# Optimization experiments

Hardware: AMD Instinct MI355X
Metric: run time of the kernel (lower is better)

The kernel has to match this reference:

```python
import jax, jax.numpy as jnp
import numpy as np

P = 10          # num_patches
EPS = 1e-20
ALPHAS = dict(stretch=1.0, E=1.0, G=1.0, skew=1.0, total_area=1.0, total_area_mult=1.0)
ALPHA_MC = 1.0
ALPHA_DISTORT = 1.0


def setup_inputs() -> dict:
    key = jax.random.key(0)
    k1, k2, k3, k4 = jax.random.split(key, 4)
    B, N, M = 8, 8192, 2500
    pc_gt = jax.random.normal(k1, (B, N, 3), dtype=jnp.float32)
    pc_pred = jax.random.normal(k2, (B, M, 3), dtype=jnp.float32)
    # first fundamental form (E, F, G); ensure E*G - F^2 > 0 so sqrt is smooth
    u = jax.random.uniform(k3, (B, M, 3), dtype=jnp.float32)
    fff = u * 0.5 + jnp.array([1.0, 0.0, 1.0], dtype=jnp.float32)
    A_gt = jax.random.uniform(k4, (B,), dtype=jnp.float32)
    return {"pc_gt": pc_gt, "pc_pred": pc_pred, "fff": fff, "A_gt": A_gt}


def _forward(pc_gt, pc_pred, fff, A_gt):
    B, M, _ = pc_pred.shape
    spp = M // P

    # ---- Chamfer distance via dense (B, M, N) distance matrix + argmin ----
    diff = pc_pred[:, :, None, :] - pc_gt[:, None, :, :]          # (B, M, N, 3)
    distm = jnp.sqrt(jnp.sum(diff * diff, axis=3))                # (B, M, N)
    inds_p2gt = jnp.argmin(distm, axis=2)                         # (B, M)
    inds_gt2p = jnp.argmin(distm, axis=1)                         # (B, N)
    pc_gt_reg = jnp.take_along_axis(pc_gt, inds_p2gt[..., None], axis=1)   # (B, M, 3)
    pc_p_reg = jnp.take_along_axis(pc_pred, inds_gt2p[..., None], axis=1)  # (B, N, 3)
    d_p2gt = jnp.sum((pc_pred - pc_gt_reg) ** 2, axis=2)
    d_gt2p = jnp.sum((pc_gt - pc_p_reg) ** 2, axis=2)
    L_chd = d_p2gt.mean() + d_gt2p.mean()

    # ---- FFF-based losses ----
    EFG = jnp.transpose(fff.reshape(B, P, spp, 3), (3, 0, 1, 2))  # (3, B, P, spp)
    E, F, G = EFG[0], EFG[1], EFG[2]

    # metric consistency between consecutive frame pairs
    Eh = E.reshape(B // 2, 2, P, spp)
    Fh = F.reshape(B // 2, 2, P, spp)
    Gh = G.reshape(B // 2, 2, P, spp)
    L_mc = ((Eh[:, 0] - Eh[:, 1]) ** 2
            + 2.0 * (Fh[:, 0] - Fh[:, 1]) ** 2
            + (Gh[:, 0] - Gh[:, 1]) ** 2).mean()

    # scaled isometry (collapse) losses
    A2 = jnp.maximum(E * G - F * F, 0.0)                          # (B, P, spp)
    A = jnp.sqrt(A2)
    inv = 1.0 / (A2 + EPS)
    L_stretch = (((E - G) ** 2) * inv).mean() * ALPHAS['stretch']
    L_E = (((E - E.mean()) ** 2) * inv).mean() * ALPHAS['E']
    L_G = (((G - G.mean()) ** 2) * inv).mean() * ALPHAS['G']
    L_F = ((F * F) * inv).mean() * ALPHAS['skew']

    # overlap / total-area loss
    A_tot = A.mean(axis=2).sum(axis=1)                            # (B,)
    L_olap = (jnp.maximum(0.0, A_tot - A_gt * ALPHAS['total_area_mult']) ** 2).mean() * ALPHAS['total_area']

    loss_sciso = L_F + L_E + L_G + L_stretch + L_olap
    loss_tot = L_chd + ALPHA_MC * L_mc + ALPHA_DISTORT * loss_sciso
    return loss_tot


def reference(pc_gt, pc_pred, fff, A_gt):
    return _forward(pc_gt, pc_pred, fff, A_gt)
```

## Files before the change

kernel.cpp:

```cpp
#include <hip/hip_runtime.h>

#define B_   8
#define N_   8192
#define M_   2500
#define SPP_ 250
#define EPS_ 1e-20f
#define BIGF 1e30f

#define NB_P2GT 320
#define NB_GT2P 256
#define NB_FFF  79
#define NB_K1   (NB_P2GT + NB_GT2P + NB_FFF)

#define NB_RG2P 256
#define NB_RP2  79
#define NB_K2   (NB_RG2P + NB_RP2)

#define WS_P2GT 0
#define WS_GT2P 160000
#define WS_ACC  291072
#define WS_RED  291092
#define WS_CNT  291427
#define A_E    0
#define A_G    1
#define A_MC   2
#define A_ST   3
#define A_F2I  4
#define A_E2I  5
#define A_EI   6
#define A_G2I  7
#define A_GI   8
#define A_I    9
#define A_AB   10
#define RO_G2P 0
#define RO_P2  256

typedef __attribute__((ext_vector_type(8))) short short8_t;
typedef __attribute__((ext_vector_type(4))) float float4_t;

__device__ __forceinline__ unsigned pack_bf2(float lo, float hi) {
    unsigned a = __float_as_uint(lo);
    unsigned b = __float_as_uint(hi);
    a = (a + 0x7FFFu + ((a >> 16) & 1u)) >> 16;
    b = (b + 0x7FFFu + ((b >> 16) & 1u)) & 0xFFFF0000u;
    return a | b;
}
__device__ __forceinline__ short bf16s(float x) {
    unsigned a = __float_as_uint(x);
    return (short)((a + 0x7FFFu + ((a >> 16) & 1u)) >> 16);
}
__device__ __forceinline__ float wave_sum64(float v) {
    #pragma unroll
    for (int o = 32; o > 0; o >>= 1) v += __shfl_down(v, o, 64);
    return v;
}
__device__ __forceinline__ float block_sum256(float v, volatile float* red4) {
    v = wave_sum64(v);
    int wid = threadIdx.x >> 6, lane = threadIdx.x & 63;
    if (lane == 0) red4[wid] = v;
    __syncthreads();
    float r = 0.f;
    if (threadIdx.x == 0) r = red4[0] + red4[1] + red4[2] + red4[3];
    __syncthreads();
    return r;
}
__device__ __forceinline__ void min4(float4_t& c, const float4_t d) {
    c.x = fminf(c.x, d.x); c.y = fminf(c.y, d.y);
    c.z = fminf(c.z, d.z); c.w = fminf(c.w, d.w);
}
__device__ __forceinline__ void quad_min4(float4_t& c) {
    #pragma unroll
    for (int m = 1; m < 16; m <<= 1) {
        c.x = fminf(c.x, __shfl_xor(c.x, m, 64));
        c.y = fminf(c.y, __shfl_xor(c.y, m, 64));
        c.z = fminf(c.z, __shfl_xor(c.z, m, 64));
        c.w = fminf(c.w, __shfl_xor(c.w, m, 64));
    }
}

__global__ void __launch_bounds__(256, 2) k1_main(
        const float* __restrict__ gt, const float* __restrict__ pred,
        const float* __restrict__ fff, float* __restrict__ ws) {
    __shared__ uint4 spts[1280];
    __shared__ __align__(16) float saux[516];
    const int bid = blockIdx.x;
    const int tid = threadIdx.x;
    const int lane = tid & 63;
    const int w    = tid >> 6;
    const int quad = lane >> 4;
    const int l15  = lane & 15;
    float* acc = ws + WS_ACC;

    if (bid == 0 && tid == 0) ((unsigned*)(ws + WS_CNT))[0] = 0u;

    if (bid < NB_P2GT + NB_GT2P) {
        const bool is_p2gt = bid < NB_P2GT;
        int b, mblk, z, ntiles, blim, alim;
        const float* apts; const float* bpts; float* dst;
        if (is_p2gt) {
            z = bid / 40; int rem = bid % 40;
            b = rem / 5;  mblk = rem % 5;
            apts = pred + (size_t)b * M_ * 3;
            bpts = gt + ((size_t)b * N_ + (size_t)z * 1024) * 3;
            ntiles = 64; blim = 1024; alim = M_;
            dst = ws + WS_P2GT + (size_t)z * 20000 + b * M_;
        } else {
            int r = bid - NB_P2GT;
            z = r >> 7; int rem = r & 127;
            b = rem >> 4; mblk = rem & 15;
            apts = gt + (size_t)b * N_ * 3;
            bpts = pred + ((size_t)b * M_ + (size_t)z * 1280) * 3;
            ntiles = 80; blim = M_ - z * 1280; alim = N_;
            dst = ws + WS_GT2P + (size_t)z * 65536 + b * N_;
        }
        const int abase = mblk * 512;
        const int nstage = ntiles * 16;

        for (int i = tid; i < nstage; i += 256) {
            float x = 0.f, y = 0.f, zc = 0.f, n2 = BIGF;
            if (i < blim) {
                x = bpts[i * 3 + 0]; y = bpts[i * 3 + 1]; zc = bpts[i * 3 + 2];
                n2 = x * x + y * y + zc * zc;
            }
            uint4 q;
            q.x = pack_bf2(-2.f * x, -2.f * y);
            q.y = pack_bf2(-2.f * zc, n2);
            q.z = q.x; q.w = q.y;
            spts[i] = q;
        }

        short8_t af[8];
        #pragma unroll
        for (int t = 0; t < 8; ++t) af[t] = (short8_t){0,0,0,0,0,0,0,0};
        if (lane < 16) {
            #pragma unroll
            for (int t = 0; t < 8; ++t) {
                int m = abase + w * 128 + t * 16 + l15;
                int c = m < alim ? m : alim - 1;
                float x = apts[c*3+0], y = apts[c*3+1], zc = apts[c*3+2];
                af[t][0] = bf16s(x); af[t][1] = bf16s(y); af[t][2] = bf16s(zc);
                af[t][3] = (short)0x3F80;
                saux[w * 128 + t * 16 + l15] = x*x + y*y + zc*zc;
            }
        }
        __syncthreads();

        const float4_t* bp = (const float4_t*)saux;
        float4_t bias[8], c[8];
        #pragma unroll
        for (int t = 0; t < 8; ++t) {
            bias[t] = bp[w * 32 + t * 4 + quad];
            c[t] = (float4_t){BIGF, BIGF, BIGF, BIGF};
        }

        const uint4* bptr = spts + l15;
        #pragma unroll 2
        for (int i = 0; i < ntiles; ++i) {
            short8_t bf = __builtin_bit_cast(short8_t, bptr[i * 16]);
            #pragma unroll
            for (int t = 0; t < 8; ++t) {
                float4_t d = __builtin_amdgcn_mfma_f32_16x16x32_bf16(
                                 af[t], bf, bias[t], 0, 0, 0);
                min4(c[t], d);
            }
        }
        #pragma unroll
        for (int t = 0; t < 8; ++t) {
            quad_min4(c[t]);
            c[t].x = fmaxf(c[t].x, 0.f); c[t].y = fmaxf(c[t].y, 0.f);
            c[t].z = fmaxf(c[t].z, 0.f); c[t].w = fmaxf(c[t].w, 0.f);
        }
        if (l15 == 0) {
            #pragma unroll
            for (int t = 0; t < 8; ++t) {
                int m0 = abase + w * 128 + t * 16 + quad * 4;
                if (m0 < alim)
                    *(float4_t*)(dst + m0) = c[t];
            }
        }
    } else {
        const int kb = bid - NB_P2GT - NB_GT2P;
        const int i  = kb * 256 + tid;
        volatile float* red4 = saux + 512;
        float* sA = saux;
        if (tid < B_) sA[tid] = 0.f;
        __syncthreads();

        float vE=0.f,vG=0.f,vMC=0.f,vST=0.f,vF2=0.f,vE2=0.f,vEI=0.f,
              vG2=0.f,vGI=0.f,vI=0.f;
        if (i < B_ * M_) {
            const int b = i / M_;
            const int m = i - b * M_;
            const float* f = fff + (size_t)i * 3;
            float E = f[0], F = f[1], G = f[2];
            float A2  = fmaxf(E * G - F * F, 0.f);
            float inv = 1.f / (A2 + EPS_);
            vE = E; vG = G;
            vST = (E - G) * (E - G) * inv;
            vF2 = F * F * inv;
            vE2 = E * E * inv; vEI = E * inv;
            vG2 = G * G * inv; vGI = G * inv;
            vI  = inv;
            atomicAdd(&sA[b], sqrtf(A2));
            if ((b & 1) == 0) {
                const float* f2 = fff + ((size_t)(b + 1) * M_ + m) * 3;
                float dE = E - f2[0], dF = F - f2[1], dG = G - f2[2];
                vMC = dE * dE + 2.f * dF * dF + dG * dG;
            }
        }
        float r;
        r = block_sum256(vE,  red4); if (tid==0) atomicAdd(&acc[A_E],   r);
        r = block_sum256(vG,  red4); if (tid==0) atomicAdd(&acc[A_G],   r);
        r = block_sum256(vMC, red4); if (tid==0) atomicAdd(&acc[A_MC],  r);
        r = block_sum256(vST, red4); if (tid==0) atomicAdd(&acc[A_ST],  r);
        r = block_sum256(vF2, red4); if (tid==0) atomicAdd(&acc[A_F2I], r);
        r = block_sum256(vE2, red4); if (tid==0) atomicAdd(&acc[A_E2I], r);
        r = block_sum256(vEI, red4); if (tid==0) atomicAdd(&acc[A_EI],  r);
        r = block_sum256(vG2, red4); if (tid==0) atomicAdd(&acc[A_G2I], r);
        r = block_sum256(vGI, red4); if (tid==0) atomicAdd(&acc[A_GI],  r);
        r = block_sum256(vI,  red4); if (tid==0) atomicAdd(&acc[A_I],   r);
        __syncthreads();
        if (tid < B_ && sA[tid] != 0.f) atomicAdd(&acc[A_AB + tid], sA[tid]);
    }
}

__global__ void __launch_bounds__(256) k2_reduce(
        const float* __restrict__ fff, const float* __restrict__ A_gt,
        float* __restrict__ ws, float* __restrict__ out) {
    __shared__ float red4[4];
    const int bid = blockIdx.x;
    const int tid = threadIdx.x;
    float* redp = ws + WS_RED;
    float* acc  = ws + WS_ACC;

    if (bid < NB_RG2P) {
        const int o = bid * 256 + tid;
        const float* src = ws + WS_GT2P + o;
        float m = fminf(src[0], src[65536]);
        float r = block_sum256(m, red4);
        if (tid == 0) redp[RO_G2P + bid] = r;
    } else {
        const int kb = bid - NB_RG2P;
        const int o = kb * 256 + tid;
        float s = 0.f;
        if (o < 20000) {
            const float* src = ws + WS_P2GT + o;
            float m = src[0];
            #pragma unroll
            for (int zz = 1; zz < 8; ++zz) m = fminf(m, src[zz * 20000]);
            s = m;
        }
        float r = block_sum256(s, red4);
        if (tid == 0) redp[RO_P2 + kb] = r;
    }

    __syncthreads();
    if (tid == 0) __threadfence();
    __syncthreads();
    __shared__ unsigned old_s;
    if (tid == 0)
        old_s = __hip_atomic_fetch_add((unsigned*)(ws + WS_CNT), 1u,
                                       __ATOMIC_ACQ_REL, __HIP_MEMORY_SCOPE_AGENT);
    __syncthreads();
    if (old_s == (unsigned)(NB_K2 - 1)) {
        float v;
        v = redp[RO_G2P + tid];
        float sGT2P = block_sum256(v, red4);
        v = (tid < 79) ? redp[RO_P2 + tid] : 0.f;
        float sP2GT = block_sum256(v, red4);
        if (tid == 0) {
            float a[18];
            #pragma unroll
            for (int k = 0; k < 18; ++k)
                a[k] = __hip_atomic_load(&acc[k], __ATOMIC_RELAXED,
                                         __HIP_MEMORY_SCOPE_AGENT);
            const float inv20k = 1.f / 20000.f;
            float mE = a[A_E] * inv20k, mG = a[A_G] * inv20k;
            float L_E = (a[A_E2I] - 2.f*mE*a[A_EI] + mE*mE*a[A_I]) * inv20k;
            float L_G = (a[A_G2I] - 2.f*mG*a[A_GI] + mG*mG*a[A_I]) * inv20k;
            float L_sc = L_E + L_G + (a[A_ST] + a[A_F2I]) * inv20k;
            float L_mc = a[A_MC] * (1.f / 10000.f);
            float L_chd = sP2GT * inv20k + sGT2P * (1.f / 65536.f);
            float L_olap = 0.f;
            #pragma unroll
            for (int b = 0; b < B_; ++b) {
                float At = a[A_AB + b] * (1.f / (float)SPP_);
                float d  = fmaxf(0.f, At - A_gt[b]);
                L_olap += d * d;
            }
            L_olap *= (1.f / (float)B_);
            out[0] = L_chd + L_mc + L_sc + L_olap;
        }
    }
}

extern "C" void kernel_launch(void* const* d_in, const int* in_sizes, int n_in,
                              void* d_out, int out_size, void* d_ws, size_t ws_size,
                              hipStream_t stream) {
    const float* pc_gt   = (const float*)d_in[0];
    const float* pc_pred = (const float*)d_in[1];
    const float* fff     = (const float*)d_in[2];
    const float* A_gt    = (const float*)d_in[3];
    float* ws  = (float*)d_ws;
    float* out = (float*)d_out;

    hipMemsetAsync(ws + WS_ACC, 0, 20 * sizeof(float), stream);
    k1_main  <<<NB_K1, 256, 0, stream>>>(pc_gt, pc_pred, fff, ws);
    k2_reduce<<<NB_K2, 256, 0, stream>>>(fff, A_gt, ws, out);
}
```

Before: 96.79 us.

## Halve per-block query tile, raise occupancy, replace atomics with per-block partials

Each distance block now handles 256 query points instead of 512, which doubles the block count and lets four blocks share a compute unit, so the GPU has more waves and better load balance. The inner loop loads two B tiles per iteration to keep the MFMA pipeline fed with fewer accumulators. The FFF loss blocks write their partial sums to per-block slots instead of using global atomics, and the final reducer sums those slots, which removes the memset launch. The cost is that every block restages the same B points into shared memory, doubling that traffic, and the final reduction does more block-wide sums.

```diff
diff --git a/kernel.cpp b/kernel.cpp
--- a/kernel.cpp
+++ b/kernel.cpp
@@ -7,8 +7,8 @@
 #define EPS_ 1e-20f
 #define BIGF 1e30f
 
-#define NB_P2GT 320
-#define NB_GT2P 256
+#define NB_P2GT 640
+#define NB_GT2P 512
 #define NB_FFF  79
 #define NB_K1   (NB_P2GT + NB_GT2P + NB_FFF)
 
@@ -18,22 +18,22 @@
 
 #define WS_P2GT 0
 #define WS_GT2P 160000
-#define WS_ACC  291072
-#define WS_RED  291092
-#define WS_CNT  291427
-#define A_E    0
-#define A_G    1
-#define A_MC   2
-#define A_ST   3
-#define A_F2I  4
-#define A_E2I  5
-#define A_EI   6
-#define A_G2I  7
-#define A_GI   8
-#define A_I    9
-#define A_AB   10
+#define WS_F1P  291072
+#define WS_RED  292968
+#define WS_CNT  293303
 #define RO_G2P 0
 #define RO_P2  256
+#define F_E    0
+#define F_G    1
+#define F_MC   2
+#define F_ST   3
+#define F_F2I  4
+#define F_E2I  5
+#define F_EI   6
+#define F_G2I  7
+#define F_GI   8
+#define F_I    9
+#define F_AB   10
 
 typedef __attribute__((ext_vector_type(8))) short short8_t;
 typedef __attribute__((ext_vector_type(4))) float float4_t;
@@ -78,18 +78,17 @@
     }
 }
 
-__global__ void __launch_bounds__(256, 2) k1_main(
+__global__ void __launch_bounds__(256, 4) k1_main(
         const float* __restrict__ gt, const float* __restrict__ pred,
         const float* __restrict__ fff, float* __restrict__ ws) {
     __shared__ uint4 spts[1280];
-    __shared__ __align__(16) float saux[516];
+    __shared__ __align__(16) float saux[264];
     const int bid = blockIdx.x;
     const int tid = threadIdx.x;
     const int lane = tid & 63;
     const int w    = tid >> 6;
     const int quad = lane >> 4;
     const int l15  = lane & 15;
-    float* acc = ws + WS_ACC;
 
     if (bid == 0 && tid == 0) ((unsigned*)(ws + WS_CNT))[0] = 0u;
 
@@ -98,22 +97,22 @@
         int b, mblk, z, ntiles, blim, alim;
         const float* apts; const float* bpts; float* dst;
         if (is_p2gt) {
-            z = bid / 40; int rem = bid % 40;
-            b = rem / 5;  mblk = rem % 5;
+            z = bid / 80; int rem = bid % 80;
+            b = rem / 10; mblk = rem % 10;
             apts = pred + (size_t)b * M_ * 3;
             bpts = gt + ((size_t)b * N_ + (size_t)z * 1024) * 3;
             ntiles = 64; blim = 1024; alim = M_;
             dst = ws + WS_P2GT + (size_t)z * 20000 + b * M_;
         } else {
             int r = bid - NB_P2GT;
-            z = r >> 7; int rem = r & 127;
-            b = rem >> 4; mblk = rem & 15;
+            z = r >> 8; int rem = r & 255;
+            b = rem >> 5; mblk = rem & 31;
             apts = gt + (size_t)b * N_ * 3;
             bpts = pred + ((size_t)b * M_ + (size_t)z * 1280) * 3;
             ntiles = 80; blim = M_ - z * 1280; alim = N_;
             dst = ws + WS_GT2P + (size_t)z * 65536 + b * N_;
         }
-        const int abase = mblk * 512;
+        const int abase = mblk * 256;
         const int nstage = ntiles * 16;
 
         for (int i = tid; i < nstage; i += 256) {
@@ -129,51 +128,59 @@
             spts[i] = q;
         }
 
-        short8_t af[8];
+        short8_t af[4];
         #pragma unroll
-        for (int t = 0; t < 8; ++t) af[t] = (short8_t){0,0,0,0,0,0,0,0};
+        for (int t = 0; t < 4; ++t) af[t] = (short8_t){0,0,0,0,0,0,0,0};
         if (lane < 16) {
             #pragma unroll
-            for (int t = 0; t < 8; ++t) {
-                int m = abase + w * 128 + t * 16 + l15;
+            for (int t = 0; t < 4; ++t) {
+                int m = abase + w * 64 + t * 16 + l15;
                 int c = m < alim ? m : alim - 1;
                 float x = apts[c*3+0], y = apts[c*3+1], zc = apts[c*3+2];
                 af[t][0] = bf16s(x); af[t][1] = bf16s(y); af[t][2] = bf16s(zc);
                 af[t][3] = (short)0x3F80;
-                saux[w * 128 + t * 16 + l15] = x*x + y*y + zc*zc;
+                saux[w * 64 + t * 16 + l15] = x*x + y*y + zc*zc;
             }
         }
         __syncthreads();
 
         const float4_t* bp = (const float4_t*)saux;
-        float4_t bias[8], c[8];
+        float4_t bias[4], c[4];
         #pragma unroll
-        for (int t = 0; t < 8; ++t) {
-            bias[t] = bp[w * 32 + t * 4 + quad];
+        for (int t = 0; t < 4; ++t) {
+            bias[t] = bp[w * 16 + t * 4 + quad];
             c[t] = (float4_t){BIGF, BIGF, BIGF, BIGF};
         }
 
         const uint4* bptr = spts + l15;
+        const int npairs = ntiles >> 1;
         #pragma unroll 2
-        for (int i = 0; i < ntiles; ++i) {
-            short8_t bf = __builtin_bit_cast(short8_t, bptr[i * 16]);
-            #pragma unroll
-            for (int t = 0; t < 8; ++t) {
+        for (int i = 0; i < npairs; ++i) {
+            short8_t bf0 = __builtin_bit_cast(short8_t, bptr[(2*i)   * 16]);
+            short8_t bf1 = __builtin_bit_cast(short8_t, bptr[(2*i+1) * 16]);
+            #pragma unroll
+            for (int t = 0; t < 4; ++t) {
                 float4_t d = __builtin_amdgcn_mfma_f32_16x16x32_bf16(
-                                 af[t], bf, bias[t], 0, 0, 0);
+                                 af[t], bf0, bias[t], 0, 0, 0);
                 min4(c[t], d);
             }
+            #pragma unroll
+            for (int t = 0; t < 4; ++t) {
+                float4_t d = __builtin_amdgcn_mfma_f32_16x16x32_bf16(
+                                 af[t], bf1, bias[t], 0, 0, 0);
+                min4(c[t], d);
+            }
         }
         #pragma unroll
-        for (int t = 0; t < 8; ++t) {
+        for (int t = 0; t < 4; ++t) {
             quad_min4(c[t]);
             c[t].x = fmaxf(c[t].x, 0.f); c[t].y = fmaxf(c[t].y, 0.f);
             c[t].z = fmaxf(c[t].z, 0.f); c[t].w = fmaxf(c[t].w, 0.f);
         }
         if (l15 == 0) {
             #pragma unroll
-            for (int t = 0; t < 8; ++t) {
-                int m0 = abase + w * 128 + t * 16 + quad * 4;
+            for (int t = 0; t < 4; ++t) {
+                int m0 = abase + w * 64 + t * 16 + quad * 4;
                 if (m0 < alim)
                     *(float4_t*)(dst + m0) = c[t];
             }
@@ -181,7 +188,7 @@
     } else {
         const int kb = bid - NB_P2GT - NB_GT2P;
         const int i  = kb * 256 + tid;
-        volatile float* red4 = saux + 512;
+        volatile float* red4 = saux + 256;
         float* sA = saux;
         if (tid < B_) sA[tid] = 0.f;
         __syncthreads();
@@ -208,19 +215,20 @@
                 vMC = dE * dE + 2.f * dF * dF + dG * dG;
             }
         }
+        float* outp = ws + WS_F1P + (size_t)kb * 24;
         float r;
-        r = block_sum256(vE,  red4); if (tid==0) atomicAdd(&acc[A_E],   r);
-        r = block_sum256(vG,  red4); if (tid==0) atomicAdd(&acc[A_G],   r);
-        r = block_sum256(vMC, red4); if (tid==0) atomicAdd(&acc[A_MC],  r);
-        r = block_sum256(vST, red4); if (tid==0) atomicAdd(&acc[A_ST],  r);
-        r = block_sum256(vF2, red4); if (tid==0) atomicAdd(&acc[A_F2I], r);
-        r = block_sum256(vE2, red4); if (tid==0) atomicAdd(&acc[A_E2I], r);
-        r = block_sum256(vEI, red4); if (tid==0) atomicAdd(&acc[A_EI],  r);
-        r = block_sum256(vG2, red4); if (tid==0) atomicAdd(&acc[A_G2I], r);
-        r = block_sum256(vGI, red4); if (tid==0) atomicAdd(&acc[A_GI],  r);
-        r = block_sum256(vI,  red4); if (tid==0) atomicAdd(&acc[A_I],   r);
+        r = block_sum256(vE,  red4); if (tid==0) outp[F_E]   = r;
+        r = block_sum256(vG,  red4); if (tid==0) outp[F_G]   = r;
+        r = block_sum256(vMC, red4); if (tid==0) outp[F_MC]  = r;
+        r = block_sum256(vST, red4); if (tid==0) outp[F_ST]  = r;
+        r = block_sum256(vF2, red4); if (tid==0) outp[F_F2I] = r;
+        r = block_sum256(vE2, red4); if (tid==0) outp[F_E2I] = r;
+        r = block_sum256(vEI, red4); if (tid==0) outp[F_EI]  = r;
+        r = block_sum256(vG2, red4); if (tid==0) outp[F_G2I] = r;
+        r = block_sum256(vGI, red4); if (tid==0) outp[F_GI]  = r;
+        r = block_sum256(vI,  red4); if (tid==0) outp[F_I]   = r;
         __syncthreads();
-        if (tid < B_ && sA[tid] != 0.f) atomicAdd(&acc[A_AB + tid], sA[tid]);
+        if (tid < B_) outp[F_AB + tid] = sA[tid];
     }
 }
 
@@ -231,7 +239,7 @@
     const int bid = blockIdx.x;
     const int tid = threadIdx.x;
     float* redp = ws + WS_RED;
-    float* acc  = ws + WS_ACC;
+    const float* f1p = ws + WS_F1P;
 
     if (bid < NB_RG2P) {
         const int o = bid * 256 + tid;
@@ -268,23 +276,24 @@
         float sGT2P = block_sum256(v, red4);
         v = (tid < 79) ? redp[RO_P2 + tid] : 0.f;
         float sP2GT = block_sum256(v, red4);
+        float a[18];
+        #pragma unroll
+        for (int k = 0; k < 18; ++k) {
+            v = (tid < 79) ? f1p[tid * 24 + k] : 0.f;
+            a[k] = block_sum256(v, red4);
+        }
         if (tid == 0) {
-            float a[18];
-            #pragma unroll
-            for (int k = 0; k < 18; ++k)
-                a[k] = __hip_atomic_load(&acc[k], __ATOMIC_RELAXED,
-                                         __HIP_MEMORY_SCOPE_AGENT);
             const float inv20k = 1.f / 20000.f;
-            float mE = a[A_E] * inv20k, mG = a[A_G] * inv20k;
-            float L_E = (a[A_E2I] - 2.f*mE*a[A_EI] + mE*mE*a[A_I]) * inv20k;
-            float L_G = (a[A_G2I] - 2.f*mG*a[A_GI] + mG*mG*a[A_I]) * inv20k;
-            float L_sc = L_E + L_G + (a[A_ST] + a[A_F2I]) * inv20k;
-            float L_mc = a[A_MC] * (1.f / 10000.f);
+            float mE = a[F_E] * inv20k, mG = a[F_G] * inv20k;
+            float L_E = (a[F_E2I] - 2.f*mE*a[F_EI] + mE*mE*a[F_I]) * inv20k;
+            float L_G = (a[F_G2I] - 2.f*mG*a[F_GI] + mG*mG*a[F_I]) * inv20k;
+            float L_sc = L_E + L_G + (a[F_ST] + a[F_F2I]) * inv20k;
+            float L_mc = a[F_MC] * (1.f / 10000.f);
             float L_chd = sP2GT * inv20k + sGT2P * (1.f / 65536.f);
             float L_olap = 0.f;
             #pragma unroll
             for (int b = 0; b < B_; ++b) {
-                float At = a[A_AB + b] * (1.f / (float)SPP_);
+                float At = a[F_AB + b] * (1.f / (float)SPP_);
                 float d  = fmaxf(0.f, At - A_gt[b]);
                 L_olap += d * d;
             }
@@ -304,7 +313,6 @@
     float* ws  = (float*)d_ws;
     float* out = (float*)d_out;
 
-    hipMemsetAsync(ws + WS_ACC, 0, 20 * sizeof(float), stream);
     k1_main  <<<NB_K1, 256, 0, stream>>>(pc_gt, pc_pred, fff, ws);
     k2_reduce<<<NB_K2, 256, 0, stream>>>(fff, A_gt, ws, out);
 }
```

New measurement: 100.9 us. +4.3%, slower.
